# Kernel tuning notes

Hardware: AMD Instinct MI355X
Metric: run time of the kernel (lower is better)

## Reference

```python
import jax, jax.numpy as jnp
import numpy as np

N_NODES = 100000
N_EDGES = 1600000
IN_DIM = 256
HIDDEN = 64


def setup_inputs() -> dict:
    key = jax.random.key(0)
    k0, k1, k2, k3 = jax.random.split(key, 4)
    x = jax.random.normal(k0, (N_NODES, IN_DIM), dtype=jnp.float32)
    edge_index = jax.random.randint(k1, (2, N_EDGES), 0, N_NODES, dtype=jnp.int64)
    # GCNConv weight [in_dim, hidden] + bias, MLP Linear(hidden, 1) + bias
    W = jax.random.normal(k2, (IN_DIM, HIDDEN), dtype=jnp.float32) * 0.05
    b = jnp.zeros((HIDDEN,), dtype=jnp.float32)
    w2 = jax.random.normal(k3, (HIDDEN, 1), dtype=jnp.float32) * 0.05
    b2 = jnp.zeros((1,), dtype=jnp.float32)
    return {"x": x, "edge_index": edge_index, "W": W, "b": b, "w2": w2, "b2": b2}


def reference(x, edge_index, W, b, w2, b2):
    N = x.shape[0]
    # PyG GCNConv default: add self-loops, symmetric normalization D^-1/2 A D^-1/2
    loops = jnp.arange(N, dtype=edge_index.dtype)
    src = jnp.concatenate([edge_index[0], loops])  # [E + N]
    dst = jnp.concatenate([edge_index[1], loops])
    h = x @ W  # [N, H] transform first (hidden < in_dim)
    deg = jax.ops.segment_sum(jnp.ones_like(dst, dtype=h.dtype), dst, num_segments=N)
    dinv = jnp.where(deg > 0, jax.lax.rsqrt(deg), 0.0)
    norm = dinv[src] * dinv[dst]  # [E + N]
    agg = jax.ops.segment_sum(h[src] * norm[:, None], dst, num_segments=N) + b  # [N, H]
    score = jax.nn.sigmoid(agg @ w2 + b2)  # [N, 1]
    return score.squeeze(-1)
```

## Files before the change

### kernel.cpp

```cpp
#include <hip/hip_runtime.h>
#include <math.h>

#define N_NODES 100000
#define N_EDGES 1600000
#define IN_DIM  256
#define HIDDEN  64

#define D_CH    32
#define D_QPB   12500
#define D_PR    4
#define D_DNR   25600
#define D_DW    6400
#define DEGB    128
#define S_CH    64
#define S_QPB   6250
#define S_SR    8
#define S_RANGE 12544

__global__ void __launch_bounds__(1024) fusedA_kernel(const float* __restrict__ x,
                                                      const float* __restrict__ W,
                                                      const float* __restrict__ w2,
                                                      const int4* __restrict__ dst4,
                                                      unsigned* __restrict__ partialD,
                                                      float* __restrict__ s) {
    __shared__ __align__(16) unsigned sh[D_DW];
    const int bid = blockIdx.x, tid = threadIdx.x;
    if (bid < DEGB) {
        const int r  = bid & (D_PR - 1);
        const int bb = bid >> 2;
        const int nbase = r * D_DNR;
        for (int i = tid; i < D_DW; i += 1024) sh[i] = 0u;
        __syncthreads();
        const int q0 = bb * D_QPB;
        for (int k = tid; k < D_QPB; k += 1024) {
            int4 d4 = dst4[q0 + k];
            int d0 = d4.x - nbase, d1 = d4.y - nbase, d2 = d4.z - nbase, d3 = d4.w - nbase;
            if ((unsigned)d0 < (unsigned)D_DNR) atomicAdd(&sh[d0 >> 2], 1u << ((d0 & 3) * 8));
            if ((unsigned)d1 < (unsigned)D_DNR) atomicAdd(&sh[d1 >> 2], 1u << ((d1 & 3) * 8));
            if ((unsigned)d2 < (unsigned)D_DNR) atomicAdd(&sh[d2 >> 2], 1u << ((d2 & 3) * 8));
            if ((unsigned)d3 < (unsigned)D_DNR) atomicAdd(&sh[d3 >> 2], 1u << ((d3 & 3) * 8));
        }
        __syncthreads();
        unsigned* outp = partialD + (size_t)bid * D_DW;
        for (int i = tid; i < D_DW; i += 1024) outp[i] = sh[i];
    } else {
        float* vsh = (float*)sh;
        if (tid < IN_DIM) {
            const float4* wr  = (const float4*)(W + tid * HIDDEN);
            const float4* w2r = (const float4*)w2;
            float acc = 0.f;
            #pragma unroll
            for (int j = 0; j < HIDDEN / 4; ++j) {
                float4 a = wr[j], q = w2r[j];
                acc += a.x * q.x + a.y * q.y + a.z * q.z + a.w * q.w;
            }
            vsh[tid] = acc;
        }
        __syncthreads();
        const int wid  = tid >> 6;
        const int lane = tid & 63;
        const int g    = lane >> 4;
        const int l16  = lane & 15;
        const float4* vr = (const float4*)vsh;
        float4 vv0 = vr[l16];
        float4 vv1 = vr[l16 + 16];
        float4 vv2 = vr[l16 + 32];
        float4 vv3 = vr[l16 + 48];
        #pragma unroll 2
        for (int n0 = ((bid - DEGB) * 16 + wid) * 4; n0 < N_NODES; n0 += 384 * 16 * 4) {
            const float4* xr = (const float4*)(x + (size_t)(n0 + g) * IN_DIM);
            float4 a0 = xr[l16];
            float4 a1 = xr[l16 + 16];
            float4 a2 = xr[l16 + 32];
            float4 a3 = xr[l16 + 48];
            float d = a0.x * vv0.x + a0.y * vv0.y + a0.z * vv0.z + a0.w * vv0.w
                    + a1.x * vv1.x + a1.y * vv1.y + a1.z * vv1.z + a1.w * vv1.w
                    + a2.x * vv2.x + a2.y * vv2.y + a2.z * vv2.z + a2.w * vv2.w
                    + a3.x * vv3.x + a3.y * vv3.y + a3.z * vv3.z + a3.w * vv3.w;
            d += __shfl_down(d, 8, 16);
            d += __shfl_down(d, 4, 16);
            d += __shfl_down(d, 2, 16);
            d += __shfl_down(d, 1, 16);
            if (l16 == 0) s[n0 + g] = d;
        }
    }
}

__global__ void deg_merge_kernel(const unsigned* __restrict__ partialD,
                                 const float* __restrict__ s,
                                 float* __restrict__ dinv, float* __restrict__ t) {
    int w = blockIdx.x * blockDim.x + threadIdx.x;
    if (w >= N_NODES / 4) return;
    const int r = w / D_DW, j = w - r * D_DW;
    unsigned a0 = 0, a1 = 0, a2 = 0, a3 = 0;
    #pragma unroll 8
    for (int bb = 0; bb < D_CH; ++bb) {
        unsigned p = partialD[(size_t)(bb * D_PR + r) * D_DW + j];
        a0 += p & 255u; a1 += (p >> 8) & 255u; a2 += (p >> 16) & 255u; a3 += p >> 24;
    }
    const int n0 = w * 4;
    float4 sv = *(const float4*)(s + n0);
    float4 di, tv;
    di.x = rsqrtf((float)(a0 + 1)); di.y = rsqrtf((float)(a1 + 1));
    di.z = rsqrtf((float)(a2 + 1)); di.w = rsqrtf((float)(a3 + 1));
    tv.x = di.x * sv.x; tv.y = di.y * sv.y; tv.z = di.z * sv.z; tv.w = di.w * sv.w;
    *(float4*)(dinv + n0) = di;
    *(float4*)(t + n0) = tv;
}

__global__ void __launch_bounds__(1024) scat_hist_kernel(const int4* __restrict__ src4,
                                                         const int4* __restrict__ dst4,
                                                         const float* __restrict__ t,
                                                         float* __restrict__ partialU) {
    __shared__ float acc[S_RANGE];
    const int r  = blockIdx.x & (S_SR - 1);
    const int bb = blockIdx.x >> 3;
    const int nbase = r * S_RANGE;
    for (int i = threadIdx.x; i < S_RANGE; i += 1024) acc[i] = 0.f;
    __syncthreads();
    const int q0 = bb * S_QPB;
    for (int k = threadIdx.x; k < S_QPB; k += 1024) {
        int4 d4 = dst4[q0 + k];
        int4 s4 = src4[q0 + k];
        int d0 = d4.x - nbase, d1 = d4.y - nbase, d2 = d4.z - nbase, d3 = d4.w - nbase;
        if ((unsigned)d0 < (unsigned)S_RANGE) atomicAdd(&acc[d0], t[s4.x]);
        if ((unsigned)d1 < (unsigned)S_RANGE) atomicAdd(&acc[d1], t[s4.y]);
        if ((unsigned)d2 < (unsigned)S_RANGE) atomicAdd(&acc[d2], t[s4.z]);
        if ((unsigned)d3 < (unsigned)S_RANGE) atomicAdd(&acc[d3], t[s4.w]);
    }
    __syncthreads();
    float* outp = partialU + (size_t)blockIdx.x * S_RANGE;
    for (int i = threadIdx.x; i < S_RANGE; i += 1024) outp[i] = acc[i];
}

__global__ void merge_final_kernel(const float* __restrict__ partialU,
                                   const float* __restrict__ dinv,
                                   const float* __restrict__ s,
                                   const float* __restrict__ b,
                                   const float* __restrict__ w2,
                                   const float* __restrict__ b2,
                                   float* __restrict__ out) {
    float c = b2[0];
    #pragma unroll 8
    for (int j = 0; j < HIDDEN; ++j) c += b[j] * w2[j];
    int g = blockIdx.x * blockDim.x + threadIdx.x;
    if (g >= N_NODES / 4) return;
    const int n0 = g * 4;
    const int r = n0 / S_RANGE, j = n0 - r * S_RANGE;
    float4 u = make_float4(0.f, 0.f, 0.f, 0.f);
    #pragma unroll 8
    for (int bl = 0; bl < S_CH; ++bl) {
        float4 p = *(const float4*)(partialU + (size_t)(bl * S_SR + r) * S_RANGE + j);
        u.x += p.x; u.y += p.y; u.z += p.z; u.w += p.w;
    }
    float4 di = *(const float4*)(dinv + n0);
    float4 sv = *(const float4*)(s + n0);
    float4 o;
    o.x = 1.f / (1.f + expf(-(di.x * (u.x + di.x * sv.x) + c)));
    o.y = 1.f / (1.f + expf(-(di.y * (u.y + di.y * sv.y) + c)));
    o.z = 1.f / (1.f + expf(-(di.z * (u.z + di.z * sv.z) + c)));
    o.w = 1.f / (1.f + expf(-(di.w * (u.w + di.w * sv.w) + c)));
    *(float4*)(out + n0) = o;
}

__global__ void wv_kernel(const float* __restrict__ W, const float* __restrict__ b,
                          const float* __restrict__ w2, const float* __restrict__ b2,
                          float* __restrict__ v, float* __restrict__ c) {
    int i = threadIdx.x;
    float acc = 0.f;
    for (int j = 0; j < HIDDEN; ++j) acc += W[i * HIDDEN + j] * w2[j];
    v[i] = acc;
    if (i == 0) {
        float cc = b2[0];
        for (int j = 0; j < HIDDEN; ++j) cc += b[j] * w2[j];
        *c = cc;
    }
}
__global__ void s_kernel(const float* __restrict__ x, const float* __restrict__ v,
                         float* __restrict__ s) {
    const int wave = threadIdx.x >> 6;
    const int lane = threadIdx.x & 63;
    const int n = blockIdx.x * 4 + wave;
    const float4* xr = (const float4*)(x + (size_t)n * IN_DIM);
    const float4* vr = (const float4*)v;
    float4 a  = xr[lane];
    float4 vv = vr[lane];
    float d = a.x * vv.x + a.y * vv.y + a.z * vv.z + a.w * vv.w;
    #pragma unroll
    for (int off = 32; off > 0; off >>= 1) d += __shfl_down(d, off, 64);
    if (lane == 0) s[n] = d;
}
__global__ void deg_kernel(const int* __restrict__ dst, int* __restrict__ cnt) {
    int e = blockIdx.x * blockDim.x + threadIdx.x;
    if (e < N_EDGES) atomicAdd(&cnt[dst[e]], 1);
}
__global__ void dinv_kernel(const int* __restrict__ cnt, const float* __restrict__ s,
                            float* __restrict__ dinv, float* __restrict__ t) {
    int n = blockIdx.x * blockDim.x + threadIdx.x;
    if (n < N_NODES) {
        float di = rsqrtf((float)(cnt[n] + 1));
        dinv[n] = di;
        t[n] = di * s[n];
    }
}
__global__ void scatter_kernel(const int* __restrict__ src, const int* __restrict__ dst,
                               const float* __restrict__ t, float* __restrict__ u) {
    int e = blockIdx.x * blockDim.x + threadIdx.x;
    if (e < N_EDGES) atomicAdd(&u[dst[e]], t[src[e]]);
}
__global__ void final_kernel(const float* __restrict__ dinv, const float* __restrict__ u,
                             const float* __restrict__ s, const float* __restrict__ c,
                             float* __restrict__ out) {
    int n = blockIdx.x * blockDim.x + threadIdx.x;
    if (n < N_NODES) {
        float di = dinv[n];
        float pre = di * (u[n] + di * s[n]) + c[0];
        out[n] = 1.f / (1.f + expf(-pre));
    }
}

extern "C" void kernel_launch(void* const* d_in, const int* in_sizes, int n_in,
                              void* d_out, int out_size, void* d_ws, size_t ws_size,
                              hipStream_t stream) {
    const float* x   = (const float*)d_in[0];
    const int*   ei  = (const int*)  d_in[1];
    const float* W   = (const float*)d_in[2];
    const float* b   = (const float*)d_in[3];
    const float* w2  = (const float*)d_in[4];
    const float* b2  = (const float*)d_in[5];
    float* out = (float*)d_out;

    const int* src = ei;
    const int* dst = ei + N_EDGES;

    float* ws = (float*)d_ws;
    float*    s        = ws + 0;
    float*    t        = ws + 100352;
    float*    dinv     = ws + 200704;
    unsigned* partialD = (unsigned*)(ws + 301056);
    float*    partialU = ws + 1120256;
    const size_t need_bytes = (size_t)(1120256 + (size_t)S_CH * S_SR * S_RANGE) * 4;

    if (ws_size >= need_bytes) {
        fusedA_kernel<<<512, 1024, 0, stream>>>(x, W, w2, (const int4*)dst, partialD, s);
        deg_merge_kernel<<<(N_NODES / 4 + 255) / 256, 256, 0, stream>>>(partialD, s, dinv, t);
        scat_hist_kernel<<<S_CH * S_SR, 1024, 0, stream>>>((const int4*)src,
                                                           (const int4*)dst, t, partialU);
        merge_final_kernel<<<(N_NODES / 4 + 255) / 256, 256, 0, stream>>>(partialU, dinv, s,
                                                                          b, w2, b2, out);
    } else {
        float* v   = ws + 0;
        float* c   = ws + 256;
        float* sf  = ws + 512;
        float* tf  = ws + 100608;
        float* df  = ws + 200704;
        float* u   = ws + 300800;
        int*   cnt = (int*)(ws + 400800);
        hipMemsetAsync((char*)d_ws + (size_t)300800 * 4, 0, (size_t)200000 * 4, stream);
        wv_kernel<<<1, 256, 0, stream>>>(W, b, w2, b2, v, c);
        s_kernel<<<N_NODES / 4, 256, 0, stream>>>(x, v, sf);
        deg_kernel<<<(N_EDGES + 255) / 256, 256, 0, stream>>>(dst, cnt);
        dinv_kernel<<<(N_NODES + 255) / 256, 256, 0, stream>>>(cnt, sf, df, tf);
        scatter_kernel<<<(N_EDGES + 255) / 256, 256, 0, stream>>>(src, dst, tf, u);
        final_kernel<<<(N_NODES + 255) / 256, 256, 0, stream>>>(df, u, sf, c, out);
    }
}
```

Baseline: 199.9 us.

## Replace privatized LDS histograms with direct global atomics for degree and scatter

Drops the per-block shared-memory partial histograms for both the degree count and the edge scatter, along with their merge passes, in favour of global atomicAdd into zeroed count and accumulator arrays. A memset is added to clear those arrays before the fused kernel runs. This removes the multi-megabyte partial buffers and the reduction reads over them. In exchange, 1.6M random global atomics now contend in L2, and float-atomic ordering makes the summation nondeterministic.

```diff
diff --git a/kernel.cpp b/kernel.cpp
--- a/kernel.cpp
+++ b/kernel.cpp
@@ -6,45 +6,28 @@
 #define IN_DIM  256
 #define HIDDEN  64
 
-#define D_CH    32
-#define D_QPB   12500
-#define D_PR    4
-#define D_DNR   25600
-#define D_DW    6400
-#define DEGB    128
-#define S_CH    64
-#define S_QPB   6250
-#define S_SR    8
-#define S_RANGE 12544
-
-__global__ void __launch_bounds__(1024) fusedA_kernel(const float* __restrict__ x,
-                                                      const float* __restrict__ W,
-                                                      const float* __restrict__ w2,
-                                                      const int4* __restrict__ dst4,
-                                                      unsigned* __restrict__ partialD,
-                                                      float* __restrict__ s) {
-    __shared__ __align__(16) unsigned sh[D_DW];
+#define DEGB   128
+#define D_QPB  3125
+#define SBLK   384
+
+__global__ void __launch_bounds__(1024) fusedA2_kernel(const float* __restrict__ x,
+                                                       const float* __restrict__ W,
+                                                       const float* __restrict__ w2,
+                                                       const int4* __restrict__ dst4,
+                                                       int* __restrict__ cnt,
+                                                       float* __restrict__ s) {
+    __shared__ __align__(16) float vsh[IN_DIM];
     const int bid = blockIdx.x, tid = threadIdx.x;
     if (bid < DEGB) {
-        const int r  = bid & (D_PR - 1);
-        const int bb = bid >> 2;
-        const int nbase = r * D_DNR;
-        for (int i = tid; i < D_DW; i += 1024) sh[i] = 0u;
-        __syncthreads();
-        const int q0 = bb * D_QPB;
+        const int q0 = bid * D_QPB;
         for (int k = tid; k < D_QPB; k += 1024) {
             int4 d4 = dst4[q0 + k];
-            int d0 = d4.x - nbase, d1 = d4.y - nbase, d2 = d4.z - nbase, d3 = d4.w - nbase;
-            if ((unsigned)d0 < (unsigned)D_DNR) atomicAdd(&sh[d0 >> 2], 1u << ((d0 & 3) * 8));
-            if ((unsigned)d1 < (unsigned)D_DNR) atomicAdd(&sh[d1 >> 2], 1u << ((d1 & 3) * 8));
-            if ((unsigned)d2 < (unsigned)D_DNR) atomicAdd(&sh[d2 >> 2], 1u << ((d2 & 3) * 8));
-            if ((unsigned)d3 < (unsigned)D_DNR) atomicAdd(&sh[d3 >> 2], 1u << ((d3 & 3) * 8));
+            atomicAdd(&cnt[d4.x], 1);
+            atomicAdd(&cnt[d4.y], 1);
+            atomicAdd(&cnt[d4.z], 1);
+            atomicAdd(&cnt[d4.w], 1);
         }
-        __syncthreads();
-        unsigned* outp = partialD + (size_t)bid * D_DW;
-        for (int i = tid; i < D_DW; i += 1024) outp[i] = sh[i];
     } else {
-        float* vsh = (float*)sh;
         if (tid < IN_DIM) {
             const float4* wr  = (const float4*)(W + tid * HIDDEN);
             const float4* w2r = (const float4*)w2;
@@ -67,7 +50,7 @@
         float4 vv2 = vr[l16 + 32];
         float4 vv3 = vr[l16 + 48];
         #pragma unroll 2
-        for (int n0 = ((bid - DEGB) * 16 + wid) * 4; n0 < N_NODES; n0 += 384 * 16 * 4) {
+        for (int n0 = ((bid - DEGB) * 16 + wid) * 4; n0 < N_NODES; n0 += SBLK * 16 * 4) {
             const float4* xr = (const float4*)(x + (size_t)(n0 + g) * IN_DIM);
             float4 a0 = xr[l16];
             float4 a1 = xr[l16 + 16];
@@ -86,81 +69,56 @@
     }
 }
 
-__global__ void deg_merge_kernel(const unsigned* __restrict__ partialD,
-                                 const float* __restrict__ s,
-                                 float* __restrict__ dinv, float* __restrict__ t) {
+__global__ void dinv_t_kernel(const int4* __restrict__ cnt4,
+                              const float* __restrict__ s,
+                              float* __restrict__ dinv, float* __restrict__ t) {
     int w = blockIdx.x * blockDim.x + threadIdx.x;
     if (w >= N_NODES / 4) return;
-    const int r = w / D_DW, j = w - r * D_DW;
-    unsigned a0 = 0, a1 = 0, a2 = 0, a3 = 0;
-    #pragma unroll 8
-    for (int bb = 0; bb < D_CH; ++bb) {
-        unsigned p = partialD[(size_t)(bb * D_PR + r) * D_DW + j];
-        a0 += p & 255u; a1 += (p >> 8) & 255u; a2 += (p >> 16) & 255u; a3 += p >> 24;
-    }
-    const int n0 = w * 4;
-    float4 sv = *(const float4*)(s + n0);
+    int4 c4 = cnt4[w];
+    float4 sv = ((const float4*)s)[w];
     float4 di, tv;
-    di.x = rsqrtf((float)(a0 + 1)); di.y = rsqrtf((float)(a1 + 1));
-    di.z = rsqrtf((float)(a2 + 1)); di.w = rsqrtf((float)(a3 + 1));
+    di.x = rsqrtf((float)(c4.x + 1)); di.y = rsqrtf((float)(c4.y + 1));
+    di.z = rsqrtf((float)(c4.z + 1)); di.w = rsqrtf((float)(c4.w + 1));
     tv.x = di.x * sv.x; tv.y = di.y * sv.y; tv.z = di.z * sv.z; tv.w = di.w * sv.w;
-    *(float4*)(dinv + n0) = di;
-    *(float4*)(t + n0) = tv;
-}
-
-__global__ void __launch_bounds__(1024) scat_hist_kernel(const int4* __restrict__ src4,
-                                                         const int4* __restrict__ dst4,
-                                                         const float* __restrict__ t,
-                                                         float* __restrict__ partialU) {
-    __shared__ float acc[S_RANGE];
-    const int r  = blockIdx.x & (S_SR - 1);
-    const int bb = blockIdx.x >> 3;
-    const int nbase = r * S_RANGE;
-    for (int i = threadIdx.x; i < S_RANGE; i += 1024) acc[i] = 0.f;
-    __syncthreads();
-    const int q0 = bb * S_QPB;
-    for (int k = threadIdx.x; k < S_QPB; k += 1024) {
-        int4 d4 = dst4[q0 + k];
-        int4 s4 = src4[q0 + k];
-        int d0 = d4.x - nbase, d1 = d4.y - nbase, d2 = d4.z - nbase, d3 = d4.w - nbase;
-        if ((unsigned)d0 < (unsigned)S_RANGE) atomicAdd(&acc[d0], t[s4.x]);
-        if ((unsigned)d1 < (unsigned)S_RANGE) atomicAdd(&acc[d1], t[s4.y]);
-        if ((unsigned)d2 < (unsigned)S_RANGE) atomicAdd(&acc[d2], t[s4.z]);
-        if ((unsigned)d3 < (unsigned)S_RANGE) atomicAdd(&acc[d3], t[s4.w]);
-    }
-    __syncthreads();
-    float* outp = partialU + (size_t)blockIdx.x * S_RANGE;
-    for (int i = threadIdx.x; i < S_RANGE; i += 1024) outp[i] = acc[i];
-}
-
-__global__ void merge_final_kernel(const float* __restrict__ partialU,
-                                   const float* __restrict__ dinv,
-                                   const float* __restrict__ s,
-                                   const float* __restrict__ b,
-                                   const float* __restrict__ w2,
-                                   const float* __restrict__ b2,
-                                   float* __restrict__ out) {
+    ((float4*)dinv)[w] = di;
+    ((float4*)t)[w] = tv;
+}
+
+__global__ void __launch_bounds__(1024) scat_atomic_kernel(const int4* __restrict__ src4,
+                                                           const int4* __restrict__ dst4,
+                                                           const float* __restrict__ t,
+                                                           float* __restrict__ u) {
+    int g = blockIdx.x * 1024 + threadIdx.x;
+    if (g >= N_EDGES / 4) return;
+    int4 d4 = dst4[g];
+    int4 s4 = src4[g];
+    atomicAdd(&u[d4.x], t[s4.x]);
+    atomicAdd(&u[d4.y], t[s4.y]);
+    atomicAdd(&u[d4.z], t[s4.z]);
+    atomicAdd(&u[d4.w], t[s4.w]);
+}
+
+__global__ void final2_kernel(const float* __restrict__ u,
+                              const float* __restrict__ dinv,
+                              const float* __restrict__ s,
+                              const float* __restrict__ b,
+                              const float* __restrict__ w2,
+                              const float* __restrict__ b2,
+                              float* __restrict__ out) {
     float c = b2[0];
     #pragma unroll 8
     for (int j = 0; j < HIDDEN; ++j) c += b[j] * w2[j];
     int g = blockIdx.x * blockDim.x + threadIdx.x;
     if (g >= N_NODES / 4) return;
-    const int n0 = g * 4;
-    const int r = n0 / S_RANGE, j = n0 - r * S_RANGE;
-    float4 u = make_float4(0.f, 0.f, 0.f, 0.f);
-    #pragma unroll 8
-    for (int bl = 0; bl < S_CH; ++bl) {
-        float4 p = *(const float4*)(partialU + (size_t)(bl * S_SR + r) * S_RANGE + j);
-        u.x += p.x; u.y += p.y; u.z += p.z; u.w += p.w;
-    }
-    float4 di = *(const float4*)(dinv + n0);
-    float4 sv = *(const float4*)(s + n0);
+    float4 uv = ((const float4*)u)[g];
+    float4 di = ((const float4*)dinv)[g];
+    float4 sv = ((const float4*)s)[g];
     float4 o;
-    o.x = 1.f / (1.f + expf(-(di.x * (u.x + di.x * sv.x) + c)));
-    o.y = 1.f / (1.f + expf(-(di.y * (u.y + di.y * sv.y) + c)));
-    o.z = 1.f / (1.f + expf(-(di.z * (u.z + di.z * sv.z) + c)));
-    o.w = 1.f / (1.f + expf(-(di.w * (u.w + di.w * sv.w) + c)));
-    *(float4*)(out + n0) = o;
+    o.x = 1.f / (1.f + expf(-(di.x * (uv.x + di.x * sv.x) + c)));
+    o.y = 1.f / (1.f + expf(-(di.y * (uv.y + di.y * sv.y) + c)));
+    o.z = 1.f / (1.f + expf(-(di.z * (uv.z + di.z * sv.z) + c)));
+    o.w = 1.f / (1.f + expf(-(di.w * (uv.w + di.w * sv.w) + c)));
+    ((float4*)out)[g] = o;
 }
 
 __global__ void wv_kernel(const float* __restrict__ W, const float* __restrict__ b,
@@ -234,34 +192,36 @@
     const int* dst = ei + N_EDGES;
 
     float* ws = (float*)d_ws;
-    float*    s        = ws + 0;
-    float*    t        = ws + 100352;
-    float*    dinv     = ws + 200704;
-    unsigned* partialD = (unsigned*)(ws + 301056);
-    float*    partialU = ws + 1120256;
-    const size_t need_bytes = (size_t)(1120256 + (size_t)S_CH * S_SR * S_RANGE) * 4;
+    float* s    = ws + 0;
+    float* t    = ws + 100352;
+    float* dinv = ws + 200704;
+    int*   cnt  = (int*)(ws + 301056);
+    float* u    = ws + 401408;
+    const size_t need_bytes = (size_t)501760 * 4;
 
     if (ws_size >= need_bytes) {
-        fusedA_kernel<<<512, 1024, 0, stream>>>(x, W, w2, (const int4*)dst, partialD, s);
-        deg_merge_kernel<<<(N_NODES / 4 + 255) / 256, 256, 0, stream>>>(partialD, s, dinv, t);
-        scat_hist_kernel<<<S_CH * S_SR, 1024, 0, stream>>>((const int4*)src,
-                                                           (const int4*)dst, t, partialU);
-        merge_final_kernel<<<(N_NODES / 4 + 255) / 256, 256, 0, stream>>>(partialU, dinv, s,
-                                                                          b, w2, b2, out);
+        hipMemsetAsync((char*)d_ws + (size_t)301056 * 4, 0, (size_t)200704 * 4, stream);
+        fusedA2_kernel<<<DEGB + SBLK, 1024, 0, stream>>>(x, W, w2, (const int4*)dst, cnt, s);
+        dinv_t_kernel<<<(N_NODES / 4 + 255) / 256, 256, 0, stream>>>((const int4*)cnt, s,
+                                                                     dinv, t);
+        scat_atomic_kernel<<<(N_EDGES / 4 + 1023) / 1024, 1024, 0, stream>>>(
+            (const int4*)src, (const int4*)dst, t, u);
+        final2_kernel<<<(N_NODES / 4 + 255) / 256, 256, 0, stream>>>(u, dinv, s,
+                                                                     b, w2, b2, out);
     } else {
         float* v   = ws + 0;
         float* c   = ws + 256;
         float* sf  = ws + 512;
         float* tf  = ws + 100608;
         float* df  = ws + 200704;
-        float* u   = ws + 300800;
-        int*   cnt = (int*)(ws + 400800);
+        float* uu  = ws + 300800;
+        int*   cn  = (int*)(ws + 400800);
         hipMemsetAsync((char*)d_ws + (size_t)300800 * 4, 0, (size_t)200000 * 4, stream);
         wv_kernel<<<1, 256, 0, stream>>>(W, b, w2, b2, v, c);
         s_kernel<<<N_NODES / 4, 256, 0, stream>>>(x, v, sf);
-        deg_kernel<<<(N_EDGES + 255) / 256, 256, 0, stream>>>(dst, cnt);
-        dinv_kernel<<<(N_NODES + 255) / 256, 256, 0, stream>>>(cnt, sf, df, tf);
-        scatter_kernel<<<(N_EDGES + 255) / 256, 256, 0, stream>>>(src, dst, tf, u);
-        final_kernel<<<(N_NODES + 255) / 256, 256, 0, stream>>>(df, u, sf, c, out);
-    }
-}
+        deg_kernel<<<(N_EDGES + 255) / 256, 256, 0, stream>>>(dst, cn);
+        dinv_kernel<<<(N_NODES + 255) / 256, 256, 0, stream>>>(cn, sf, df, tf);
+        scatter_kernel<<<(N_EDGES + 255) / 256, 256, 0, stream>>>(src, dst, tf, uu);
+        final_kernel<<<(N_NODES + 255) / 256, 256, 0, stream>>>(df, uu, sf, c, out);
+    }
+}
```

Measured after the change: 290.2 us. +45.2%, slower.

## Fuse four kernels into one persistent kernel with software grid barriers

Applied to the files above, without the earlier changes.

Merges the four launched kernels into a single persistent kernel of 512 blocks that are separated by atomic-counter grid barriers, which removes the per-launch overhead and the tail gaps between launches. The final merge now splits each group of four nodes across eight threads and combines them with shuffles, which adds parallelism to the partial-sum reduction. The barriers assume all 512 blocks of 1024 threads are resident at the same time. That holds only under the occupancy requested by launch bounds, and if it fails the kernel deadlocks. A memset of the barrier counters is added per call.

```diff
diff --git a/kernel.cpp b/kernel.cpp
--- a/kernel.cpp
+++ b/kernel.cpp
@@ -6,45 +6,70 @@
 #define IN_DIM  256
 #define HIDDEN  64
 
+#define NB      512
+#define DEGB    128
 #define D_CH    32
 #define D_QPB   12500
 #define D_PR    4
 #define D_DNR   25600
 #define D_DW    6400
-#define DEGB    128
+#define SBLK    384
 #define S_CH    64
 #define S_QPB   6250
 #define S_SR    8
 #define S_RANGE 12544
 
-__global__ void __launch_bounds__(1024) fusedA_kernel(const float* __restrict__ x,
-                                                      const float* __restrict__ W,
-                                                      const float* __restrict__ w2,
-                                                      const int4* __restrict__ dst4,
-                                                      unsigned* __restrict__ partialD,
-                                                      float* __restrict__ s) {
-    __shared__ __align__(16) unsigned sh[D_DW];
+__device__ __forceinline__ void grid_barrier(int* cnt, int* flag, int target) {
+    __syncthreads();
+    if (threadIdx.x == 0) {
+        __threadfence();
+        if (__hip_atomic_fetch_add(cnt, 1, __ATOMIC_ACQ_REL, __HIP_MEMORY_SCOPE_AGENT)
+            == NB - 1) {
+            __hip_atomic_store(cnt, 0, __ATOMIC_RELAXED, __HIP_MEMORY_SCOPE_AGENT);
+            __hip_atomic_fetch_add(flag, 1, __ATOMIC_RELEASE, __HIP_MEMORY_SCOPE_AGENT);
+        } else {
+            while (__hip_atomic_load(flag, __ATOMIC_ACQUIRE, __HIP_MEMORY_SCOPE_AGENT)
+                   < target) {
+                __builtin_amdgcn_s_sleep(2);
+            }
+        }
+    }
+    __syncthreads();
+}
+
+__global__ void __launch_bounds__(1024, 8) mono_kernel(
+    const float* __restrict__ x, const float* __restrict__ W,
+    const float* __restrict__ w2, const float* __restrict__ b,
+    const float* __restrict__ b2,
+    const int4* __restrict__ src4, const int4* __restrict__ dst4,
+    unsigned* __restrict__ partialD, float* __restrict__ partialU,
+    float* __restrict__ s, float* __restrict__ t, float* __restrict__ dinv,
+    int* __restrict__ bar, float* __restrict__ out)
+{
+    __shared__ __align__(16) float smem[S_RANGE];
     const int bid = blockIdx.x, tid = threadIdx.x;
+
     if (bid < DEGB) {
+        unsigned* hist = (unsigned*)smem;
         const int r  = bid & (D_PR - 1);
         const int bb = bid >> 2;
         const int nbase = r * D_DNR;
-        for (int i = tid; i < D_DW; i += 1024) sh[i] = 0u;
+        for (int i = tid; i < D_DW; i += 1024) hist[i] = 0u;
         __syncthreads();
         const int q0 = bb * D_QPB;
         for (int k = tid; k < D_QPB; k += 1024) {
             int4 d4 = dst4[q0 + k];
             int d0 = d4.x - nbase, d1 = d4.y - nbase, d2 = d4.z - nbase, d3 = d4.w - nbase;
-            if ((unsigned)d0 < (unsigned)D_DNR) atomicAdd(&sh[d0 >> 2], 1u << ((d0 & 3) * 8));
-            if ((unsigned)d1 < (unsigned)D_DNR) atomicAdd(&sh[d1 >> 2], 1u << ((d1 & 3) * 8));
-            if ((unsigned)d2 < (unsigned)D_DNR) atomicAdd(&sh[d2 >> 2], 1u << ((d2 & 3) * 8));
-            if ((unsigned)d3 < (unsigned)D_DNR) atomicAdd(&sh[d3 >> 2], 1u << ((d3 & 3) * 8));
+            if ((unsigned)d0 < (unsigned)D_DNR) atomicAdd(&hist[d0 >> 2], 1u << ((d0 & 3) * 8));
+            if ((unsigned)d1 < (unsigned)D_DNR) atomicAdd(&hist[d1 >> 2], 1u << ((d1 & 3) * 8));
+            if ((unsigned)d2 < (unsigned)D_DNR) atomicAdd(&hist[d2 >> 2], 1u << ((d2 & 3) * 8));
+            if ((unsigned)d3 < (unsigned)D_DNR) atomicAdd(&hist[d3 >> 2], 1u << ((d3 & 3) * 8));
         }
         __syncthreads();
         unsigned* outp = partialD + (size_t)bid * D_DW;
-        for (int i = tid; i < D_DW; i += 1024) outp[i] = sh[i];
+        for (int i = tid; i < D_DW; i += 1024) outp[i] = hist[i];
     } else {
-        float* vsh = (float*)sh;
+        float* vsh = smem;
         if (tid < IN_DIM) {
             const float4* wr  = (const float4*)(W + tid * HIDDEN);
             const float4* w2r = (const float4*)w2;
@@ -67,7 +92,7 @@
         float4 vv2 = vr[l16 + 32];
         float4 vv3 = vr[l16 + 48];
         #pragma unroll 2
-        for (int n0 = ((bid - DEGB) * 16 + wid) * 4; n0 < N_NODES; n0 += 384 * 16 * 4) {
+        for (int n0 = ((bid - DEGB) * 16 + wid) * 4; n0 < N_NODES; n0 += SBLK * 16 * 4) {
             const float4* xr = (const float4*)(x + (size_t)(n0 + g) * IN_DIM);
             float4 a0 = xr[l16];
             float4 a1 = xr[l16 + 16];
@@ -84,83 +109,97 @@
             if (l16 == 0) s[n0 + g] = d;
         }
     }
-}
-
-__global__ void deg_merge_kernel(const unsigned* __restrict__ partialD,
-                                 const float* __restrict__ s,
-                                 float* __restrict__ dinv, float* __restrict__ t) {
-    int w = blockIdx.x * blockDim.x + threadIdx.x;
-    if (w >= N_NODES / 4) return;
-    const int r = w / D_DW, j = w - r * D_DW;
-    unsigned a0 = 0, a1 = 0, a2 = 0, a3 = 0;
-    #pragma unroll 8
-    for (int bb = 0; bb < D_CH; ++bb) {
-        unsigned p = partialD[(size_t)(bb * D_PR + r) * D_DW + j];
-        a0 += p & 255u; a1 += (p >> 8) & 255u; a2 += (p >> 16) & 255u; a3 += p >> 24;
-    }
-    const int n0 = w * 4;
-    float4 sv = *(const float4*)(s + n0);
-    float4 di, tv;
-    di.x = rsqrtf((float)(a0 + 1)); di.y = rsqrtf((float)(a1 + 1));
-    di.z = rsqrtf((float)(a2 + 1)); di.w = rsqrtf((float)(a3 + 1));
-    tv.x = di.x * sv.x; tv.y = di.y * sv.y; tv.z = di.z * sv.z; tv.w = di.w * sv.w;
-    *(float4*)(dinv + n0) = di;
-    *(float4*)(t + n0) = tv;
-}
-
-__global__ void __launch_bounds__(1024) scat_hist_kernel(const int4* __restrict__ src4,
-                                                         const int4* __restrict__ dst4,
-                                                         const float* __restrict__ t,
-                                                         float* __restrict__ partialU) {
-    __shared__ float acc[S_RANGE];
-    const int r  = blockIdx.x & (S_SR - 1);
-    const int bb = blockIdx.x >> 3;
-    const int nbase = r * S_RANGE;
-    for (int i = threadIdx.x; i < S_RANGE; i += 1024) acc[i] = 0.f;
-    __syncthreads();
-    const int q0 = bb * S_QPB;
-    for (int k = threadIdx.x; k < S_QPB; k += 1024) {
-        int4 d4 = dst4[q0 + k];
-        int4 s4 = src4[q0 + k];
-        int d0 = d4.x - nbase, d1 = d4.y - nbase, d2 = d4.z - nbase, d3 = d4.w - nbase;
-        if ((unsigned)d0 < (unsigned)S_RANGE) atomicAdd(&acc[d0], t[s4.x]);
-        if ((unsigned)d1 < (unsigned)S_RANGE) atomicAdd(&acc[d1], t[s4.y]);
-        if ((unsigned)d2 < (unsigned)S_RANGE) atomicAdd(&acc[d2], t[s4.z]);
-        if ((unsigned)d3 < (unsigned)S_RANGE) atomicAdd(&acc[d3], t[s4.w]);
-    }
-    __syncthreads();
-    float* outp = partialU + (size_t)blockIdx.x * S_RANGE;
-    for (int i = threadIdx.x; i < S_RANGE; i += 1024) outp[i] = acc[i];
-}
-
-__global__ void merge_final_kernel(const float* __restrict__ partialU,
-                                   const float* __restrict__ dinv,
-                                   const float* __restrict__ s,
-                                   const float* __restrict__ b,
-                                   const float* __restrict__ w2,
-                                   const float* __restrict__ b2,
-                                   float* __restrict__ out) {
-    float c = b2[0];
-    #pragma unroll 8
-    for (int j = 0; j < HIDDEN; ++j) c += b[j] * w2[j];
-    int g = blockIdx.x * blockDim.x + threadIdx.x;
-    if (g >= N_NODES / 4) return;
-    const int n0 = g * 4;
-    const int r = n0 / S_RANGE, j = n0 - r * S_RANGE;
-    float4 u = make_float4(0.f, 0.f, 0.f, 0.f);
-    #pragma unroll 8
-    for (int bl = 0; bl < S_CH; ++bl) {
-        float4 p = *(const float4*)(partialU + (size_t)(bl * S_SR + r) * S_RANGE + j);
-        u.x += p.x; u.y += p.y; u.z += p.z; u.w += p.w;
-    }
-    float4 di = *(const float4*)(dinv + n0);
-    float4 sv = *(const float4*)(s + n0);
-    float4 o;
-    o.x = 1.f / (1.f + expf(-(di.x * (u.x + di.x * sv.x) + c)));
-    o.y = 1.f / (1.f + expf(-(di.y * (u.y + di.y * sv.y) + c)));
-    o.z = 1.f / (1.f + expf(-(di.z * (u.z + di.z * sv.z) + c)));
-    o.w = 1.f / (1.f + expf(-(di.w * (u.w + di.w * sv.w) + c)));
-    *(float4*)(out + n0) = o;
+    grid_barrier(bar, bar + 1, 1);
+
+    {
+        const int w = bid * 1024 + tid;
+        if (w < N_NODES / 4) {
+            const int r = w / D_DW, j = w - r * D_DW;
+            unsigned a0 = 0, a1 = 0, a2 = 0, a3 = 0;
+            #pragma unroll 8
+            for (int bb = 0; bb < D_CH; ++bb) {
+                unsigned p = partialD[(size_t)(bb * D_PR + r) * D_DW + j];
+                a0 += p & 255u; a1 += (p >> 8) & 255u;
+                a2 += (p >> 16) & 255u; a3 += p >> 24;
+            }
+            const int n0 = w * 4;
+            float4 sv = *(const float4*)(s + n0);
+            float4 di, tv;
+            di.x = rsqrtf((float)(a0 + 1)); di.y = rsqrtf((float)(a1 + 1));
+            di.z = rsqrtf((float)(a2 + 1)); di.w = rsqrtf((float)(a3 + 1));
+            tv.x = di.x * sv.x; tv.y = di.y * sv.y;
+            tv.z = di.z * sv.z; tv.w = di.w * sv.w;
+            *(float4*)(dinv + n0) = di;
+            *(float4*)(t + n0) = tv;
+        }
+    }
+    grid_barrier(bar, bar + 1, 2);
+
+    {
+        float* acc = smem;
+        const int r  = bid & (S_SR - 1);
+        const int bb = bid >> 3;
+        const int nbase = r * S_RANGE;
+        for (int i = tid; i < S_RANGE; i += 1024) acc[i] = 0.f;
+        __syncthreads();
+        const int q0 = bb * S_QPB;
+        for (int k = tid; k < S_QPB; k += 1024) {
+            int4 d4 = dst4[q0 + k];
+            int4 s4 = src4[q0 + k];
+            int d0 = d4.x - nbase, d1 = d4.y - nbase, d2 = d4.z - nbase, d3 = d4.w - nbase;
+            if ((unsigned)d0 < (unsigned)S_RANGE) atomicAdd(&acc[d0], t[s4.x]);
+            if ((unsigned)d1 < (unsigned)S_RANGE) atomicAdd(&acc[d1], t[s4.y]);
+            if ((unsigned)d2 < (unsigned)S_RANGE) atomicAdd(&acc[d2], t[s4.z]);
+            if ((unsigned)d3 < (unsigned)S_RANGE) atomicAdd(&acc[d3], t[s4.w]);
+        }
+        __syncthreads();
+        float* outp = partialU + (size_t)bid * S_RANGE;
+        for (int i = tid; i < S_RANGE; i += 1024) outp[i] = acc[i];
+    }
+    grid_barrier(bar, bar + 1, 3);
+
+    {
+        float c = b2[0];
+        #pragma unroll 8
+        for (int j = 0; j < HIDDEN; ++j) c += b[j] * w2[j];
+        const int gid = bid * 1024 + tid;
+        const int w = gid >> 3, p = gid & 7;
+        if (w < 25088) {
+            const int n0 = w * 4;
+            const int r = n0 / S_RANGE, j = n0 - r * S_RANGE;
+            float4 u = make_float4(0.f, 0.f, 0.f, 0.f);
+            #pragma unroll
+            for (int q = 0; q < 8; ++q) {
+                float4 pp = *(const float4*)(partialU
+                              + (size_t)((p + 8 * q) * S_SR + r) * S_RANGE + j);
+                u.x += pp.x; u.y += pp.y; u.z += pp.z; u.w += pp.w;
+            }
+            #pragma unroll
+            for (int off = 4; off > 0; off >>= 1) {
+                u.x += __shfl_down(u.x, off, 8);
+                u.y += __shfl_down(u.y, off, 8);
+                u.z += __shfl_down(u.z, off, 8);
+                u.w += __shfl_down(u.w, off, 8);
+            }
+            if (p == 0) {
+                float4 di = *(const float4*)(dinv + n0);
+                float4 sv = *(const float4*)(s + n0);
+                float4 o;
+                o.x = 1.f / (1.f + expf(-(di.x * (u.x + di.x * sv.x) + c)));
+                o.y = 1.f / (1.f + expf(-(di.y * (u.y + di.y * sv.y) + c)));
+                o.z = 1.f / (1.f + expf(-(di.z * (u.z + di.z * sv.z) + c)));
+                o.w = 1.f / (1.f + expf(-(di.w * (u.w + di.w * sv.w) + c)));
+                if (n0 + 3 < N_NODES) {
+                    *(float4*)(out + n0) = o;
+                } else {
+                    if (n0 + 0 < N_NODES) out[n0 + 0] = o.x;
+                    if (n0 + 1 < N_NODES) out[n0 + 1] = o.y;
+                    if (n0 + 2 < N_NODES) out[n0 + 2] = o.z;
+                    if (n0 + 3 < N_NODES) out[n0 + 3] = o.w;
+                }
+            }
+        }
+    }
 }
 
 __global__ void wv_kernel(const float* __restrict__ W, const float* __restrict__ b,
@@ -234,34 +273,37 @@
     const int* dst = ei + N_EDGES;
 
     float* ws = (float*)d_ws;
-    float*    s        = ws + 0;
-    float*    t        = ws + 100352;
-    float*    dinv     = ws + 200704;
-    unsigned* partialD = (unsigned*)(ws + 301056);
-    float*    partialU = ws + 1120256;
-    const size_t need_bytes = (size_t)(1120256 + (size_t)S_CH * S_SR * S_RANGE) * 4;
+    int*      bar      = (int*)ws;
+    float*    s        = ws + 128;
+    float*    t        = ws + 100480;
+    float*    dinv     = ws + 200832;
+    unsigned* partialD = (unsigned*)(ws + 301184);
+    float*    partialU = ws + 1120384;
+    const size_t need_bytes = (size_t)7542912 * 4;
 
     if (ws_size >= need_bytes) {
-        fusedA_kernel<<<512, 1024, 0, stream>>>(x, W, w2, (const int4*)dst, partialD, s);
-        deg_merge_kernel<<<(N_NODES / 4 + 255) / 256, 256, 0, stream>>>(partialD, s, dinv, t);
-        scat_hist_kernel<<<S_CH * S_SR, 1024, 0, stream>>>((const int4*)src,
-                                                           (const int4*)dst, t, partialU);
-        merge_final_kernel<<<(N_NODES / 4 + 255) / 256, 256, 0, stream>>>(partialU, dinv, s,
-                                                                          b, w2, b2, out);
+        hipMemsetAsync(d_ws, 0, 8, stream);
+        void* args[] = {(void*)&x, (void*)&W, (void*)&w2, (void*)&b, (void*)&b2,
+                        (void*)&src, (void*)&dst, (void*)&partialD, (void*)&partialU,
+                        (void*)&s, (void*)&t, (void*)&dinv, (void*)&bar, (void*)&out};
+        (void)args;
+        mono_kernel<<<NB, 1024, 0, stream>>>(x, W, w2, b, b2,
+                                             (const int4*)src, (const int4*)dst,
+                                             partialD, partialU, s, t, dinv, bar, out);
     } else {
         float* v   = ws + 0;
         float* c   = ws + 256;
         float* sf  = ws + 512;
         float* tf  = ws + 100608;
         float* df  = ws + 200704;
-        float* u   = ws + 300800;
-        int*   cnt = (int*)(ws + 400800);
+        float* uu  = ws + 300800;
+        int*   cn  = (int*)(ws + 400800);
         hipMemsetAsync((char*)d_ws + (size_t)300800 * 4, 0, (size_t)200000 * 4, stream);
         wv_kernel<<<1, 256, 0, stream>>>(W, b, w2, b2, v, c);
         s_kernel<<<N_NODES / 4, 256, 0, stream>>>(x, v, sf);
-        deg_kernel<<<(N_EDGES + 255) / 256, 256, 0, stream>>>(dst, cnt);
-        dinv_kernel<<<(N_NODES + 255) / 256, 256, 0, stream>>>(cnt, sf, df, tf);
-        scatter_kernel<<<(N_EDGES + 255) / 256, 256, 0, stream>>>(src, dst, tf, u);
-        final_kernel<<<(N_NODES + 255) / 256, 256, 0, stream>>>(df, u, sf, c, out);
-    }
-}
+        deg_kernel<<<(N_EDGES + 255) / 256, 256, 0, stream>>>(dst, cn);
+        dinv_kernel<<<(N_NODES + 255) / 256, 256, 0, stream>>>(cn, sf, df, tf);
+        scatter_kernel<<<(N_EDGES + 255) / 256, 256, 0, stream>>>(src, dst, tf, uu);
+        final_kernel<<<(N_NODES + 255) / 256, 256, 0, stream>>>(df, uu, sf, c, out);
+    }
+}
```

Result: slower. 436.1 us (+118.2%).

## Use atomic work-stealing for x·v rows and split merge reduction across lanes

Applied to the files above, without the earlier changes.

The fused kernel now has every block, including the degree-histogram blocks, join the x·v dot-product work once its histogram is done. Work is handed out in 64-row chunks through a global atomic counter, which the host zeroes with a memset before each launch. This removes the static split that left the 128 histogram blocks idle during the x-bandwidth phase. The merge kernel now spreads each group's 64 partial sums over 8 lanes and reduces them with shuffles, giving it more parallelism and memory-level concurrency. In exchange it adds a per-chunk atomic, two block barriers per chunk and an extra memset launch.

```diff
diff --git a/kernel.cpp b/kernel.cpp
--- a/kernel.cpp
+++ b/kernel.cpp
@@ -6,69 +6,82 @@
 #define IN_DIM  256
 #define HIDDEN  64
 
+#define NB      512
+#define DEGB    128
 #define D_CH    32
 #define D_QPB   12500
 #define D_PR    4
 #define D_DNR   25600
 #define D_DW    6400
-#define DEGB    128
+#define NCHUNK  1563
 #define S_CH    64
 #define S_QPB   6250
 #define S_SR    8
 #define S_RANGE 12544
 
-__global__ void __launch_bounds__(1024) fusedA_kernel(const float* __restrict__ x,
-                                                      const float* __restrict__ W,
-                                                      const float* __restrict__ w2,
-                                                      const int4* __restrict__ dst4,
-                                                      unsigned* __restrict__ partialD,
-                                                      float* __restrict__ s) {
-    __shared__ __align__(16) unsigned sh[D_DW];
+__global__ void __launch_bounds__(1024) fusedA5_kernel(const float* __restrict__ x,
+                                                       const float* __restrict__ W,
+                                                       const float* __restrict__ w2,
+                                                       const int4* __restrict__ dst4,
+                                                       unsigned* __restrict__ partialD,
+                                                       float* __restrict__ s,
+                                                       int* __restrict__ wcnt) {
+    __shared__ __align__(16) unsigned hist[D_DW];
+    __shared__ __align__(16) float vsh[IN_DIM];
+    __shared__ int chunk_sh;
     const int bid = blockIdx.x, tid = threadIdx.x;
+
+    if (tid < IN_DIM) {
+        const float4* wr  = (const float4*)(W + tid * HIDDEN);
+        const float4* w2r = (const float4*)w2;
+        float acc = 0.f;
+        #pragma unroll
+        for (int j = 0; j < HIDDEN / 4; ++j) {
+            float4 a = wr[j], q = w2r[j];
+            acc += a.x * q.x + a.y * q.y + a.z * q.z + a.w * q.w;
+        }
+        vsh[tid] = acc;
+    }
+
     if (bid < DEGB) {
         const int r  = bid & (D_PR - 1);
         const int bb = bid >> 2;
         const int nbase = r * D_DNR;
-        for (int i = tid; i < D_DW; i += 1024) sh[i] = 0u;
+        for (int i = tid; i < D_DW; i += 1024) hist[i] = 0u;
         __syncthreads();
         const int q0 = bb * D_QPB;
         for (int k = tid; k < D_QPB; k += 1024) {
             int4 d4 = dst4[q0 + k];
             int d0 = d4.x - nbase, d1 = d4.y - nbase, d2 = d4.z - nbase, d3 = d4.w - nbase;
-            if ((unsigned)d0 < (unsigned)D_DNR) atomicAdd(&sh[d0 >> 2], 1u << ((d0 & 3) * 8));
-            if ((unsigned)d1 < (unsigned)D_DNR) atomicAdd(&sh[d1 >> 2], 1u << ((d1 & 3) * 8));
-            if ((unsigned)d2 < (unsigned)D_DNR) atomicAdd(&sh[d2 >> 2], 1u << ((d2 & 3) * 8));
-            if ((unsigned)d3 < (unsigned)D_DNR) atomicAdd(&sh[d3 >> 2], 1u << ((d3 & 3) * 8));
+            if ((unsigned)d0 < (unsigned)D_DNR) atomicAdd(&hist[d0 >> 2], 1u << ((d0 & 3) * 8));
+            if ((unsigned)d1 < (unsigned)D_DNR) atomicAdd(&hist[d1 >> 2], 1u << ((d1 & 3) * 8));
+            if ((unsigned)d2 < (unsigned)D_DNR) atomicAdd(&hist[d2 >> 2], 1u << ((d2 & 3) * 8));
+            if ((unsigned)d3 < (unsigned)D_DNR) atomicAdd(&hist[d3 >> 2], 1u << ((d3 & 3) * 8));
         }
         __syncthreads();
         unsigned* outp = partialD + (size_t)bid * D_DW;
-        for (int i = tid; i < D_DW; i += 1024) outp[i] = sh[i];
-    } else {
-        float* vsh = (float*)sh;
-        if (tid < IN_DIM) {
-            const float4* wr  = (const float4*)(W + tid * HIDDEN);
-            const float4* w2r = (const float4*)w2;
-            float acc = 0.f;
-            #pragma unroll
-            for (int j = 0; j < HIDDEN / 4; ++j) {
-                float4 a = wr[j], q = w2r[j];
-                acc += a.x * q.x + a.y * q.y + a.z * q.z + a.w * q.w;
-            }
-            vsh[tid] = acc;
-        }
+        for (int i = tid; i < D_DW; i += 1024) outp[i] = hist[i];
+    }
+    __syncthreads();
+
+    const int wid  = tid >> 6;
+    const int lane = tid & 63;
+    const int g    = lane >> 4;
+    const int l16  = lane & 15;
+    const float4* vr = (const float4*)vsh;
+    float4 vv0 = vr[l16];
+    float4 vv1 = vr[l16 + 16];
+    float4 vv2 = vr[l16 + 32];
+    float4 vv3 = vr[l16 + 48];
+    for (;;) {
+        if (tid == 0) chunk_sh = atomicAdd(wcnt, 1);
         __syncthreads();
-        const int wid  = tid >> 6;
-        const int lane = tid & 63;
-        const int g    = lane >> 4;
-        const int l16  = lane & 15;
-        const float4* vr = (const float4*)vsh;
-        float4 vv0 = vr[l16];
-        float4 vv1 = vr[l16 + 16];
-        float4 vv2 = vr[l16 + 32];
-        float4 vv3 = vr[l16 + 48];
-        #pragma unroll 2
-        for (int n0 = ((bid - DEGB) * 16 + wid) * 4; n0 < N_NODES; n0 += 384 * 16 * 4) {
-            const float4* xr = (const float4*)(x + (size_t)(n0 + g) * IN_DIM);
+        const int c = chunk_sh;
+        __syncthreads();
+        if (c >= NCHUNK) break;
+        const int n0 = c * 64 + wid * 4 + g;
+        if (n0 < N_NODES) {
+            const float4* xr = (const float4*)(x + (size_t)n0 * IN_DIM);
             float4 a0 = xr[l16];
             float4 a1 = xr[l16 + 16];
             float4 a2 = xr[l16 + 32];
@@ -81,7 +94,7 @@
             d += __shfl_down(d, 4, 16);
             d += __shfl_down(d, 2, 16);
             d += __shfl_down(d, 1, 16);
-            if (l16 == 0) s[n0 + g] = d;
+            if (l16 == 0) s[n0] = d;
         }
     }
 }
@@ -143,24 +156,42 @@
     float c = b2[0];
     #pragma unroll 8
     for (int j = 0; j < HIDDEN; ++j) c += b[j] * w2[j];
-    int g = blockIdx.x * blockDim.x + threadIdx.x;
-    if (g >= N_NODES / 4) return;
-    const int n0 = g * 4;
+    const int gid = blockIdx.x * blockDim.x + threadIdx.x;
+    const int w = gid >> 3, p = gid & 7;
+    if (w >= 25088) return;
+    const int n0 = w * 4;
     const int r = n0 / S_RANGE, j = n0 - r * S_RANGE;
     float4 u = make_float4(0.f, 0.f, 0.f, 0.f);
-    #pragma unroll 8
-    for (int bl = 0; bl < S_CH; ++bl) {
-        float4 p = *(const float4*)(partialU + (size_t)(bl * S_SR + r) * S_RANGE + j);
-        u.x += p.x; u.y += p.y; u.z += p.z; u.w += p.w;
-    }
-    float4 di = *(const float4*)(dinv + n0);
-    float4 sv = *(const float4*)(s + n0);
-    float4 o;
-    o.x = 1.f / (1.f + expf(-(di.x * (u.x + di.x * sv.x) + c)));
-    o.y = 1.f / (1.f + expf(-(di.y * (u.y + di.y * sv.y) + c)));
-    o.z = 1.f / (1.f + expf(-(di.z * (u.z + di.z * sv.z) + c)));
-    o.w = 1.f / (1.f + expf(-(di.w * (u.w + di.w * sv.w) + c)));
-    *(float4*)(out + n0) = o;
+    #pragma unroll
+    for (int q = 0; q < 8; ++q) {
+        float4 pp = *(const float4*)(partialU
+                      + (size_t)((p + 8 * q) * S_SR + r) * S_RANGE + j);
+        u.x += pp.x; u.y += pp.y; u.z += pp.z; u.w += pp.w;
+    }
+    #pragma unroll
+    for (int off = 4; off > 0; off >>= 1) {
+        u.x += __shfl_down(u.x, off, 8);
+        u.y += __shfl_down(u.y, off, 8);
+        u.z += __shfl_down(u.z, off, 8);
+        u.w += __shfl_down(u.w, off, 8);
+    }
+    if (p == 0) {
+        float4 di = *(const float4*)(dinv + n0);
+        float4 sv = *(const float4*)(s + n0);
+        float4 o;
+        o.x = 1.f / (1.f + expf(-(di.x * (u.x + di.x * sv.x) + c)));
+        o.y = 1.f / (1.f + expf(-(di.y * (u.y + di.y * sv.y) + c)));
+        o.z = 1.f / (1.f + expf(-(di.z * (u.z + di.z * sv.z) + c)));
+        o.w = 1.f / (1.f + expf(-(di.w * (u.w + di.w * sv.w) + c)));
+        if (n0 + 3 < N_NODES) {
+            *(float4*)(out + n0) = o;
+        } else {
+            if (n0 + 0 < N_NODES) out[n0 + 0] = o.x;
+            if (n0 + 1 < N_NODES) out[n0 + 1] = o.y;
+            if (n0 + 2 < N_NODES) out[n0 + 2] = o.z;
+            if (n0 + 3 < N_NODES) out[n0 + 3] = o.w;
+        }
+    }
 }
 
 __global__ void wv_kernel(const float* __restrict__ W, const float* __restrict__ b,
@@ -234,34 +265,36 @@
     const int* dst = ei + N_EDGES;
 
     float* ws = (float*)d_ws;
-    float*    s        = ws + 0;
-    float*    t        = ws + 100352;
-    float*    dinv     = ws + 200704;
-    unsigned* partialD = (unsigned*)(ws + 301056);
-    float*    partialU = ws + 1120256;
-    const size_t need_bytes = (size_t)(1120256 + (size_t)S_CH * S_SR * S_RANGE) * 4;
+    int*      wcnt     = (int*)ws;
+    float*    s        = ws + 128;
+    float*    t        = ws + 100480;
+    float*    dinv     = ws + 200832;
+    unsigned* partialD = (unsigned*)(ws + 301184);
+    float*    partialU = ws + 1120384;
+    const size_t need_bytes = (size_t)7542912 * 4;
 
     if (ws_size >= need_bytes) {
-        fusedA_kernel<<<512, 1024, 0, stream>>>(x, W, w2, (const int4*)dst, partialD, s);
+        hipMemsetAsync(d_ws, 0, 4, stream);
+        fusedA5_kernel<<<NB, 1024, 0, stream>>>(x, W, w2, (const int4*)dst,
+                                                partialD, s, wcnt);
         deg_merge_kernel<<<(N_NODES / 4 + 255) / 256, 256, 0, stream>>>(partialD, s, dinv, t);
         scat_hist_kernel<<<S_CH * S_SR, 1024, 0, stream>>>((const int4*)src,
                                                            (const int4*)dst, t, partialU);
-        merge_final_kernel<<<(N_NODES / 4 + 255) / 256, 256, 0, stream>>>(partialU, dinv, s,
-                                                                          b, w2, b2, out);
+        merge_final_kernel<<<784, 256, 0, stream>>>(partialU, dinv, s, b, w2, b2, out);
     } else {
         float* v   = ws + 0;
         float* c   = ws + 256;
         float* sf  = ws + 512;
         float* tf  = ws + 100608;
         float* df  = ws + 200704;
-        float* u   = ws + 300800;
-        int*   cnt = (int*)(ws + 400800);
+        float* uu  = ws + 300800;
+        int*   cn  = (int*)(ws + 400800);
         hipMemsetAsync((char*)d_ws + (size_t)300800 * 4, 0, (size_t)200000 * 4, stream);
         wv_kernel<<<1, 256, 0, stream>>>(W, b, w2, b2, v, c);
         s_kernel<<<N_NODES / 4, 256, 0, stream>>>(x, v, sf);
-        deg_kernel<<<(N_EDGES + 255) / 256, 256, 0, stream>>>(dst, cnt);
-        dinv_kernel<<<(N_NODES + 255) / 256, 256, 0, stream>>>(cnt, sf, df, tf);
-        scatter_kernel<<<(N_EDGES + 255) / 256, 256, 0, stream>>>(src, dst, tf, u);
-        final_kernel<<<(N_NODES + 255) / 256, 256, 0, stream>>>(df, u, sf, c, out);
-    }
-}
+        deg_kernel<<<(N_EDGES + 255) / 256, 256, 0, stream>>>(dst, cn);
+        dinv_kernel<<<(N_NODES + 255) / 256, 256, 0, stream>>>(cn, sf, df, tf);
+        scatter_kernel<<<(N_EDGES + 255) / 256, 256, 0, stream>>>(src, dst, tf, uu);
+        final_kernel<<<(N_NODES + 255) / 256, 256, 0, stream>>>(df, uu, sf, c, out);
+    }
+}
```

New measurement: 202.3 us. About the same (+1.2%).
